# Kernel optimization log

Hardware: AMD Instinct MI355X
Metric: run time of the kernel (lower is better)

Reference implementation:

```python
import jax, jax.numpy as jnp
import numpy as np


def setup_inputs() -> dict:
    key = jax.random.key(0)
    k1, k2 = jax.random.split(key)
    B, N, F, K = 8, 8192, 128, 512
    x = jax.random.normal(k1, (B, N, F), dtype=jnp.float32)
    cluster_centers = jax.random.normal(k2, (K, F), dtype=jnp.float32)
    return {"x": x, "cluster_centers": cluster_centers}


def reference(x, cluster_centers):
    # same math as sqrt(sum((x - c)^2)) without the [B,N,K,F] intermediate).
    x_sq = jnp.sum(x * x, axis=-1, keepdims=True)                 # [B, N, 1]
    c_sq = jnp.sum(cluster_centers * cluster_centers, axis=-1)    # [K]
    cross = jnp.einsum("bnf,kf->bnk", x, cluster_centers)         # [B, N, K]
    d2 = jnp.maximum(x_sq + c_sq[None, None, :] - 2.0 * cross, 0.0)
    distances = jnp.sqrt(d2)                                      # [B, N, K]
    associations = jax.nn.softmax(-distances, axis=-1)            # [B, N, K]
    output = jnp.einsum("bnk,kf->bnf", associations, cluster_centers)
    return output
```

## Files before the change

### kernel.cpp

```cpp
#include <hip/hip_runtime.h>
#include <hip/hip_bf16.h>

typedef short v8s __attribute__((ext_vector_type(8)));
typedef float v16f __attribute__((ext_vector_type(16)));
typedef unsigned v2u __attribute__((ext_vector_type(2)));

#define F_ 128
#define K_ 512
#define M_ 65536
#define CH_SH 17408
#define CB_OFF 9216

typedef __attribute__((address_space(1))) const char gch;
typedef __attribute__((address_space(3))) char lch;

__device__ __forceinline__ short f2bf(float f) {
    union { float f; unsigned u; } v; v.f = f;
    unsigned u = v.u;
    u = (u + 0x7FFFu + ((u >> 16) & 1u)) >> 16;
    return (short)u;
}
__device__ __forceinline__ float bf2f(short s) {
    union { float f; unsigned u; } v;
    v.u = ((unsigned)(unsigned short)s) << 16;
    return v.f;
}

#if __has_builtin(__builtin_amdgcn_permlane32_swap)
#define HAVE_PLS 1
#endif

__device__ __forceinline__ void pswap(unsigned &a, unsigned &b, int lane) {
#ifdef HAVE_PLS
    v2u r = __builtin_amdgcn_permlane32_swap(a, b, false, false);
    a = (unsigned)r.x; b = (unsigned)r.y;
#else
    unsigned sa = (unsigned)__shfl_xor((int)a, 32);
    unsigned sb = (unsigned)__shfl_xor((int)b, 32);
    if (lane & 32) a = sb; else b = sa;
#endif
}

__global__ void prep_kernel(const float* __restrict__ centers, short* __restrict__ G) {
    const int c = blockIdx.x;
    const int f = threadIdx.x;
    const int ch = c >> 6, c64 = c & 63;
    const size_t base = (size_t)ch * CH_SH;
    float v = centers[c * F_ + f];
    short b = f2bf(v);
    float vb = bf2f(b);
    { const int ks = f >> 4, h = (f >> 3) & 1, j = f & 7;
      G[base + (size_t)((ks * 2 + h) * 64 + c64) * 8 + j] = b; }
    { const int kap = c64 >> 4, hh = (c64 >> 3) & 1, jj = c64 & 7;
      G[base + CB_OFF + (size_t)((kap * 2 + hh) * F_ + f) * 8 + jj] = b; }
    float s = vb * vb;
    #pragma unroll
    for (int off = 1; off < 64; off <<= 1) s += __shfl_xor(s, off);
    __shared__ float part[2];
    if ((f & 63) == 0) part[f >> 6] = s;
    __syncthreads();
    if (f < 16) {
        const float csq = part[0] + part[1];
        const float chv = -0.5f * csq;
        const short vh = f2bf(chv);
        const short vl = f2bf(chv - bf2f(vh));
        const short val = (f == 0) ? vh : (f == 1) ? vl : (f == 2) ? (short)0x3F80 : (short)0;
        const int h2 = f >> 3, j2 = f & 7;
        G[base + (size_t)((16 + h2) * 64 + c64) * 8 + j2] = val;
    }
}

__device__ __forceinline__ void stage_chunk(const short* __restrict__ G, short* dst,
                                            int ch, int wave, int lane) {
    const char* src = (const char*)(G + (size_t)ch * CH_SH);
    lch* d = (lch*)dst;
    #pragma unroll
    for (int t = 0; t < 8; ++t) {
        const int g = t * 256 + wave * 64 + lane;
        __builtin_amdgcn_global_load_lds((gch*)(src + (size_t)g * 16),
                                         d + (size_t)(t * 256 + wave * 64) * 16, 16, 0, 0);
    }
    if (wave < 2) {
        const int g = 2048 + wave * 64 + lane;
        __builtin_amdgcn_global_load_lds((gch*)(src + (size_t)g * 16),
                                         d + (size_t)(2048 + wave * 64) * 16, 16, 0, 0);
    }
}

__global__ __launch_bounds__(256, 2) void cluster_kernel(
        const float* __restrict__ x, const short* __restrict__ G,
        float* __restrict__ out) {
    __shared__ __align__(16) short SB[2][CH_SH];
    const int tid = threadIdx.x;
    const int wave = tid >> 6, lane = tid & 63;
    const int h = lane >> 5, c32 = lane & 31;
    const int row0 = blockIdx.x * 128 + wave * 32;

    short* const SB0 = &SB[0][0];
    const int off = blockIdx.x & 7;
    stage_chunk(G, SB0, off, wave, lane);

    const float4* xr4 = (const float4*)(x + (size_t)(row0 + c32) * F_);
    float4 xl[16];
    #pragma unroll
    for (int ks = 0; ks < 8; ++ks) {
        xl[2 * ks]     = xr4[ks * 4 + h * 2];
        xl[2 * ks + 1] = xr4[ks * 4 + h * 2 + 1];
    }
    v8s Bx[9];
    float xs = 0.f;
    #pragma unroll
    for (int ks = 0; ks < 8; ++ks) {
        float vv[8] = {xl[2*ks].x, xl[2*ks].y, xl[2*ks].z, xl[2*ks].w,
                       xl[2*ks+1].x, xl[2*ks+1].y, xl[2*ks+1].z, xl[2*ks+1].w};
        v8s fr;
        #pragma unroll
        for (int j = 0; j < 8; ++j) {
            short bb = f2bf(vv[j]);
            fr[j] = bb;
            float r = bf2f(bb);
            xs += r * r;
        }
        Bx[ks] = fr;
    }
    xs += __shfl_xor(xs, 32);
    {
        const float xh = -0.5f * xs;
        const short sxh = f2bf(xh);
        const short sxl = f2bf(xh - bf2f(sxh));
        v8s e = (v8s){0, 0, 0, 0, 0, 0, 0, 0};
        if (h == 0) { e[0] = (short)0x3F80; e[1] = (short)0x3F80; e[2] = sxh; e[3] = sxl; }
        Bx[8] = e;
    }

    v16f Of[4];
    #pragma unroll
    for (int ft = 0; ft < 4; ++ft)
        #pragma unroll
        for (int e2 = 0; e2 < 16; ++e2) Of[ft][e2] = 0.f;
    float lden = 0.f;

    #pragma unroll 1
    for (int j = 0; j < 8; ++j) {
        __syncthreads();
        if (j < 7)
            stage_chunk(G, SB0 + (size_t)((j + 1) & 1) * CH_SH, (off + j + 1) & 7, wave, lane);
        const short* CbS = SB0 + (size_t)(j & 1) * CH_SH;
        const short* CTS = CbS + CB_OFF;

        v16f a0, a1;
        #pragma unroll
        for (int e2 = 0; e2 < 16; ++e2) { a0[e2] = 0.f; a1[e2] = 0.f; }
        {
            v8s f0a = *(const v8s*)&CbS[(size_t)((0 * 2 + h) * 64 + c32) * 8];
            v8s f1a = *(const v8s*)&CbS[(size_t)((0 * 2 + h) * 64 + 32 + c32) * 8];
            v8s f0b = *(const v8s*)&CbS[(size_t)((1 * 2 + h) * 64 + c32) * 8];
            v8s f1b = *(const v8s*)&CbS[(size_t)((1 * 2 + h) * 64 + 32 + c32) * 8];
            #pragma unroll
            for (int ks = 0; ks < 9; ++ks) {
                v8s c0 = f0a, c1 = f1a;
                f0a = f0b; f1a = f1b;
                if (ks < 7) {
                    f0b = *(const v8s*)&CbS[(size_t)(((ks + 2) * 2 + h) * 64 + c32) * 8];
                    f1b = *(const v8s*)&CbS[(size_t)(((ks + 2) * 2 + h) * 64 + 32 + c32) * 8];
                }
                a0 = __builtin_amdgcn_mfma_f32_32x32x16_bf16(c0, Bx[ks], a0, 0, 0, 0);
                a1 = __builtin_amdgcn_mfma_f32_32x32x16_bf16(c1, Bx[ks], a1, 0, 0, 0);
            }
        }

        #pragma unroll
        for (int ct = 0; ct < 2; ++ct) {
            v8s cf[8];
            #pragma unroll
            for (int kp = 0; kp < 2; ++kp)
                #pragma unroll
                for (int ft = 0; ft < 4; ++ft)
                    cf[kp * 4 + ft] = *(const v8s*)
                        &CTS[(size_t)(((ct * 2 + kp) * 2 + h) * F_ + ft * 32 + c32) * 8];
            const v16f acc = ct ? a1 : a0;
            unsigned U[8];
            #pragma unroll
            for (int t = 0; t < 8; ++t) {
                const float d20 = fmaxf(-2.0f * acc[2 * t], 0.f);
                const float d21 = fmaxf(-2.0f * acc[2 * t + 1], 0.f);
                const float p0 = __expf(-__builtin_amdgcn_sqrtf(d20));
                const float p1 = __expf(-__builtin_amdgcn_sqrtf(d21));
                union { __hip_bfloat162 hh; unsigned u; } cv;
                cv.hh = __float22bfloat162_rn(make_float2(p0, p1));
                U[t] = cv.u;
                lden += __uint_as_float(cv.u << 16);
                lden += __uint_as_float(cv.u & 0xffff0000u);
            }
            #pragma unroll
            for (int kp = 0; kp < 2; ++kp) {
                unsigned s0 = U[4 * kp],     s2 = U[4 * kp + 2];
                unsigned s1 = U[4 * kp + 1], s3 = U[4 * kp + 3];
                pswap(s0, s2, lane);
                pswap(s1, s3, lane);
                union { v8s v; unsigned u[4]; } pf;
                pf.u[0] = s0; pf.u[1] = s1; pf.u[2] = s2; pf.u[3] = s3;
                #pragma unroll
                for (int ft = 0; ft < 4; ++ft)
                    Of[ft] = __builtin_amdgcn_mfma_f32_32x32x16_bf16(pf.v, cf[kp * 4 + ft], Of[ft], 0, 0, 0);
            }
        }
    }

    lden += __shfl_xor(lden, 32);
    const float inv = 1.0f / lden;
    float invr[16];
    #pragma unroll
    for (int r = 0; r < 16; ++r)
        invr[r] = __shfl(inv, (r & 3) + 8 * (r >> 2) + 4 * h);
    #pragma unroll
    for (int ft = 0; ft < 4; ++ft)
        #pragma unroll
        for (int r = 0; r < 16; ++r) {
            const int xrow = (r & 3) + 8 * (r >> 2) + 4 * h;
            out[(size_t)(row0 + xrow) * F_ + ft * 32 + c32] = Of[ft][r] * invr[r];
        }
}

extern "C" void kernel_launch(void* const* d_in, const int* in_sizes, int n_in,
                              void* d_out, int out_size, void* d_ws, size_t ws_size,
                              hipStream_t stream) {
    const float* x       = (const float*)d_in[0];
    const float* centers = (const float*)d_in[1];
    float* out = (float*)d_out;
    short* G = (short*)d_ws;
    prep_kernel<<<K_, F_, 0, stream>>>(centers, G);
    cluster_kernel<<<M_ / 128, 256, 0, stream>>>(x, G, out);
}
```

Measured before the change: 104.2 us.

## Split cluster chunks across wave pairs, read centers from global, reduce via LDS

Doubles the block to 512 threads so two waves share each 32-row tile, each handling half of the eight center chunks, then combines the partial outputs and denominators through shared memory. It drops the double-buffered LDS staging of center chunks with global_load_lds and instead has each wave read center fragments directly from global memory, relying on L2/L1 caching. This aims to raise parallelism and occupancy and to remove per-chunk barriers. In exchange every wave issues its own global loads, each x row is loaded and converted twice, and a final LDS reduction adds a barrier.

```diff
diff --git a/kernel.cpp b/kernel.cpp
--- a/kernel.cpp
+++ b/kernel.cpp
@@ -10,9 +10,6 @@
 #define M_ 65536
 #define CH_SH 17408
 #define CB_OFF 9216
-
-typedef __attribute__((address_space(1))) const char gch;
-typedef __attribute__((address_space(3))) char lch;
 
 __device__ __forceinline__ short f2bf(float f) {
     union { float f; unsigned u; } v; v.f = f;
@@ -70,35 +67,73 @@
     }
 }
 
-__device__ __forceinline__ void stage_chunk(const short* __restrict__ G, short* dst,
-                                            int ch, int wave, int lane) {
-    const char* src = (const char*)(G + (size_t)ch * CH_SH);
-    lch* d = (lch*)dst;
+__device__ __forceinline__ void stage1(const short* __restrict__ CbS, const v8s* Bx,
+                                       v16f& a0, v16f& a1, int h, int c32) {
+    #pragma unroll
+    for (int e2 = 0; e2 < 16; ++e2) { a0[e2] = 0.f; a1[e2] = 0.f; }
+    v8s f0a = *(const v8s*)&CbS[(size_t)((0 * 2 + h) * 64 + c32) * 8];
+    v8s f1a = *(const v8s*)&CbS[(size_t)((0 * 2 + h) * 64 + 32 + c32) * 8];
+    v8s f0b = *(const v8s*)&CbS[(size_t)((1 * 2 + h) * 64 + c32) * 8];
+    v8s f1b = *(const v8s*)&CbS[(size_t)((1 * 2 + h) * 64 + 32 + c32) * 8];
+    #pragma unroll
+    for (int ks = 0; ks < 9; ++ks) {
+        v8s c0 = f0a, c1 = f1a;
+        f0a = f0b; f1a = f1b;
+        if (ks < 7) {
+            f0b = *(const v8s*)&CbS[(size_t)(((ks + 2) * 2 + h) * 64 + c32) * 8];
+            f1b = *(const v8s*)&CbS[(size_t)(((ks + 2) * 2 + h) * 64 + 32 + c32) * 8];
+        }
+        a0 = __builtin_amdgcn_mfma_f32_32x32x16_bf16(c0, Bx[ks], a0, 0, 0, 0);
+        a1 = __builtin_amdgcn_mfma_f32_32x32x16_bf16(c1, Bx[ks], a1, 0, 0, 0);
+    }
+}
+
+__device__ __forceinline__ void epi_ct(const v16f acc, const short* __restrict__ CTS, int ct,
+                                       float& lden, v16f (&Of)[4], int h, int c32, int lane) {
+    v8s cf[8];
+    #pragma unroll
+    for (int kp = 0; kp < 2; ++kp)
+        #pragma unroll
+        for (int ft = 0; ft < 4; ++ft)
+            cf[kp * 4 + ft] = *(const v8s*)
+                &CTS[(size_t)(((ct * 2 + kp) * 2 + h) * F_ + ft * 32 + c32) * 8];
+    unsigned U[8];
     #pragma unroll
     for (int t = 0; t < 8; ++t) {
-        const int g = t * 256 + wave * 64 + lane;
-        __builtin_amdgcn_global_load_lds((gch*)(src + (size_t)g * 16),
-                                         d + (size_t)(t * 256 + wave * 64) * 16, 16, 0, 0);
-    }
-    if (wave < 2) {
-        const int g = 2048 + wave * 64 + lane;
-        __builtin_amdgcn_global_load_lds((gch*)(src + (size_t)g * 16),
-                                         d + (size_t)(2048 + wave * 64) * 16, 16, 0, 0);
-    }
-}
-
-__global__ __launch_bounds__(256, 2) void cluster_kernel(
+        const float d20 = fmaxf(-2.0f * acc[2 * t], 0.f);
+        const float d21 = fmaxf(-2.0f * acc[2 * t + 1], 0.f);
+        const float p0 = __expf(-__builtin_amdgcn_sqrtf(d20));
+        const float p1 = __expf(-__builtin_amdgcn_sqrtf(d21));
+        union { __hip_bfloat162 hh; unsigned u; } cv;
+        cv.hh = __float22bfloat162_rn(make_float2(p0, p1));
+        U[t] = cv.u;
+        lden += __uint_as_float(cv.u << 16);
+        lden += __uint_as_float(cv.u & 0xffff0000u);
+    }
+    #pragma unroll
+    for (int kp = 0; kp < 2; ++kp) {
+        unsigned s0 = U[4 * kp],     s2 = U[4 * kp + 2];
+        unsigned s1 = U[4 * kp + 1], s3 = U[4 * kp + 3];
+        pswap(s0, s2, lane);
+        pswap(s1, s3, lane);
+        union { v8s v; unsigned u[4]; } pf;
+        pf.u[0] = s0; pf.u[1] = s1; pf.u[2] = s2; pf.u[3] = s3;
+        #pragma unroll
+        for (int ft = 0; ft < 4; ++ft)
+            Of[ft] = __builtin_amdgcn_mfma_f32_32x32x16_bf16(pf.v, cf[kp * 4 + ft], Of[ft], 0, 0, 0);
+    }
+}
+
+__global__ __launch_bounds__(512, 4) void cluster_kernel(
         const float* __restrict__ x, const short* __restrict__ G,
         float* __restrict__ out) {
-    __shared__ __align__(16) short SB[2][CH_SH];
+    __shared__ float MB[4][65][64];
     const int tid = threadIdx.x;
     const int wave = tid >> 6, lane = tid & 63;
+    const int s = wave & 1, p = wave >> 1;
     const int h = lane >> 5, c32 = lane & 31;
-    const int row0 = blockIdx.x * 128 + wave * 32;
-
-    short* const SB0 = &SB[0][0];
+    const int row0 = blockIdx.x * 128 + p * 32;
     const int off = blockIdx.x & 7;
-    stage_chunk(G, SB0, off, wave, lane);
 
     const float4* xr4 = (const float4*)(x + (size_t)(row0 + c32) * F_);
     float4 xl[16];
@@ -140,72 +175,32 @@
         for (int e2 = 0; e2 < 16; ++e2) Of[ft][e2] = 0.f;
     float lden = 0.f;
 
-    #pragma unroll 1
-    for (int j = 0; j < 8; ++j) {
-        __syncthreads();
-        if (j < 7)
-            stage_chunk(G, SB0 + (size_t)((j + 1) & 1) * CH_SH, (off + j + 1) & 7, wave, lane);
-        const short* CbS = SB0 + (size_t)(j & 1) * CH_SH;
-        const short* CTS = CbS + CB_OFF;
-
+    #pragma unroll
+    for (int j = 0; j < 4; ++j) {
+        const int ch = (off + s * 4 + j) & 7;
+        const short* Cb = G + (size_t)ch * CH_SH;
         v16f a0, a1;
-        #pragma unroll
-        for (int e2 = 0; e2 < 16; ++e2) { a0[e2] = 0.f; a1[e2] = 0.f; }
-        {
-            v8s f0a = *(const v8s*)&CbS[(size_t)((0 * 2 + h) * 64 + c32) * 8];
-            v8s f1a = *(const v8s*)&CbS[(size_t)((0 * 2 + h) * 64 + 32 + c32) * 8];
-            v8s f0b = *(const v8s*)&CbS[(size_t)((1 * 2 + h) * 64 + c32) * 8];
-            v8s f1b = *(const v8s*)&CbS[(size_t)((1 * 2 + h) * 64 + 32 + c32) * 8];
+        stage1(Cb, Bx, a0, a1, h, c32);
+        epi_ct(a0, Cb + CB_OFF, 0, lden, Of, h, c32, lane);
+        epi_ct(a1, Cb + CB_OFF, 1, lden, Of, h, c32, lane);
+    }
+
+    if (s == 1) {
+        #pragma unroll
+        for (int ft = 0; ft < 4; ++ft)
             #pragma unroll
-            for (int ks = 0; ks < 9; ++ks) {
-                v8s c0 = f0a, c1 = f1a;
-                f0a = f0b; f1a = f1b;
-                if (ks < 7) {
-                    f0b = *(const v8s*)&CbS[(size_t)(((ks + 2) * 2 + h) * 64 + c32) * 8];
-                    f1b = *(const v8s*)&CbS[(size_t)(((ks + 2) * 2 + h) * 64 + 32 + c32) * 8];
-                }
-                a0 = __builtin_amdgcn_mfma_f32_32x32x16_bf16(c0, Bx[ks], a0, 0, 0, 0);
-                a1 = __builtin_amdgcn_mfma_f32_32x32x16_bf16(c1, Bx[ks], a1, 0, 0, 0);
-            }
-        }
-
-        #pragma unroll
-        for (int ct = 0; ct < 2; ++ct) {
-            v8s cf[8];
-            #pragma unroll
-            for (int kp = 0; kp < 2; ++kp)
-                #pragma unroll
-                for (int ft = 0; ft < 4; ++ft)
-                    cf[kp * 4 + ft] = *(const v8s*)
-                        &CTS[(size_t)(((ct * 2 + kp) * 2 + h) * F_ + ft * 32 + c32) * 8];
-            const v16f acc = ct ? a1 : a0;
-            unsigned U[8];
-            #pragma unroll
-            for (int t = 0; t < 8; ++t) {
-                const float d20 = fmaxf(-2.0f * acc[2 * t], 0.f);
-                const float d21 = fmaxf(-2.0f * acc[2 * t + 1], 0.f);
-                const float p0 = __expf(-__builtin_amdgcn_sqrtf(d20));
-                const float p1 = __expf(-__builtin_amdgcn_sqrtf(d21));
-                union { __hip_bfloat162 hh; unsigned u; } cv;
-                cv.hh = __float22bfloat162_rn(make_float2(p0, p1));
-                U[t] = cv.u;
-                lden += __uint_as_float(cv.u << 16);
-                lden += __uint_as_float(cv.u & 0xffff0000u);
-            }
-            #pragma unroll
-            for (int kp = 0; kp < 2; ++kp) {
-                unsigned s0 = U[4 * kp],     s2 = U[4 * kp + 2];
-                unsigned s1 = U[4 * kp + 1], s3 = U[4 * kp + 3];
-                pswap(s0, s2, lane);
-                pswap(s1, s3, lane);
-                union { v8s v; unsigned u[4]; } pf;
-                pf.u[0] = s0; pf.u[1] = s1; pf.u[2] = s2; pf.u[3] = s3;
-                #pragma unroll
-                for (int ft = 0; ft < 4; ++ft)
-                    Of[ft] = __builtin_amdgcn_mfma_f32_32x32x16_bf16(pf.v, cf[kp * 4 + ft], Of[ft], 0, 0, 0);
-            }
-        }
-    }
+            for (int e2 = 0; e2 < 16; ++e2)
+                MB[p][ft * 16 + e2][lane] = Of[ft][e2];
+        MB[p][64][lane] = lden;
+    }
+    __syncthreads();
+    if (s == 1) return;
+    #pragma unroll
+    for (int ft = 0; ft < 4; ++ft)
+        #pragma unroll
+        for (int e2 = 0; e2 < 16; ++e2)
+            Of[ft][e2] += MB[p][ft * 16 + e2][lane];
+    lden += MB[p][64][lane];
 
     lden += __shfl_xor(lden, 32);
     const float inv = 1.0f / lden;
@@ -230,5 +225,5 @@
     float* out = (float*)d_out;
     short* G = (short*)d_ws;
     prep_kernel<<<K_, F_, 0, stream>>>(centers, G);
-    cluster_kernel<<<M_ / 128, 256, 0, stream>>>(x, G, out);
-}
+    cluster_kernel<<<M_ / 128, 512, 0, stream>>>(x, G, out);
+}
```

Result: slower. 180.8 us (+73.5%).
